# Kernel optimization log

Measured on AMD Instinct MI355X. Metric: run time of the kernel, lower is better.

## Reference

```python
import jax, jax.numpy as jnp
import numpy as np

B, T, N, H = 4, 10, 4096, 32
SR = 1.0  # sample_rate


def setup_inputs() -> dict:
    key = jax.random.key(0)
    ks = jax.random.split(key, 10)
    inputs = jax.random.normal(ks[0], (B, T, N), jnp.float32)
    states = jax.random.normal(ks[1], (T, B, N * H), jnp.float32) * 0.1
    dtw = jax.random.uniform(ks[2], (N, N), dtype=jnp.float32)
    spec_lap = jax.random.uniform(ks[3], (N, N), dtype=jnp.float32)
    laplacian = jax.random.uniform(ks[4], (N, N), dtype=jnp.float32)
    time_delay = jax.random.uniform(ks[5], (N, N), dtype=jnp.float32) * T
    W1 = jax.random.normal(ks[6], (H + 1, 2 * H), jnp.float32) * 0.05
    b1 = jnp.ones((2 * H,), jnp.float32)  # bias_init 1.0 for gate conv
    W2 = jax.random.normal(ks[7], (H + 1, H), jnp.float32) * 0.05
    b2 = jnp.zeros((H,), jnp.float32)
    return dict(inputs=inputs, states=states, dtw=dtw, spec_lap=spec_lap,
                laplacian=laplacian, time_delay=time_delay,
                W1=W1, b1=b1, W2=W2, b2=b2)


def _graph_conv(A, x, h, W, b):
    # x: [B,N], h: [B,N*H], A: [N,N] -> [B, N*out]
    conc = jnp.concatenate([x[:, :, None], h.reshape(B, N, H)], axis=2)  # [B,N,H+1]
    ac = jnp.einsum('mn,bnk->bmk', A, conc)                              # [B,N,H+1]
    out = ac @ W + b                                                     # [B,N,out]
    return out.reshape(B, -1)


def reference(inputs, states, dtw, spec_lap, laplacian, time_delay, W1, b1, W2, b2):
    eye = jnp.eye(N, dtype=jnp.float32)
    td = jnp.ceil(jnp.abs(time_delay) / SR)
    time_indicator = jnp.float32(T) - td  # tm - td with tm = times

    def step(carry, xs):
        gcn1, gcn2, _ = carry
        t, x_t, h_t = xs
        # time-based masking of dtw entries
        dtwt = jnp.where((dtw != 0) & (t + 1.0 > time_indicator), dtw, 0.0)
        multi = t == jnp.float32(T - 1)
        A = jnp.where(multi,
                      (dtwt + eye + laplacian + spec_lap) / 3.0,
                      (dtwt + spec_lap + eye) / 2.0)
        gcn1 = gcn1 + _graph_conv(A, x_t, h_t, W1, b1)       # [B, N*2H] (accumulated)
        ru = jax.nn.sigmoid(gcn1)
        r, u = jnp.split(ru, 2, axis=1)                      # flat split, as torch.chunk
        gcn2 = gcn2 + _graph_conv(A, x_t, r * h_t, W2, b2)   # [B, N*H]
        c = jnp.tanh(gcn2)
        h_new = u * h_t + (1.0 - u) * c
        return (gcn1, gcn2, h_new), None

    gcn1_0 = jnp.zeros((B, N * 2 * H), jnp.float32)
    gcn2_0 = jnp.zeros((B, N * H), jnp.float32)
    h0 = jnp.zeros((B, N * H), jnp.float32)
    ts = jnp.arange(T, dtype=jnp.float32)
    xs = (ts, jnp.transpose(inputs, (1, 0, 2)), states)  # per-step (t, x_t[B,N], h_t[B,N*H])
    (_, _, h_new), _ = jax.lax.scan(step, (gcn1_0, gcn2_0, h0), xs)
    return h_new  # [B, N*H]
```

## Files before the change

kernel.cpp:

```cpp
#include <hip/hip_runtime.h>
#include <math.h>

#define BB 4
#define TT 10
#define NN 4096
#define HH 32
#define JP 144
#define NJ2 (NN*JP)
#define NH (NN*HH)
#define NPAIR (NN*NN/2)

typedef __attribute__((ext_vector_type(8))) short short8;
typedef __attribute__((ext_vector_type(8))) _Float16 half8;
typedef __attribute__((ext_vector_type(4))) float floatx4;
typedef __attribute__((ext_vector_type(4))) unsigned int uintx4;
typedef __attribute__((ext_vector_type(2))) unsigned int uintx2;

__device__ inline unsigned short f2h(float f) {
    _Float16 h = (_Float16)f;
    unsigned short u; __builtin_memcpy(&u, &h, 2);
    return u;
}
__device__ inline unsigned pk2(float a, float b) {
    return (unsigned)f2h(a) | ((unsigned)f2h(b) << 16);
}

__global__ void k_pack(const float* __restrict__ dtw, const float* __restrict__ tdl,
                       const float* __restrict__ spl, const float* __restrict__ lap,
                       unsigned* __restrict__ Aoff, unsigned* __restrict__ Aon,
                       unsigned* __restrict__ A9, unsigned short* __restrict__ thr2) {
    int e = blockIdx.x * 256 + threadIdx.x;
    if (e >= NPAIR) return;
    size_t gi = (size_t)e * 2;
    int row = (int)(gi >> 12);
    int c0 = (int)(gi & 4095);
    float2 d = ((const float2*)dtw)[e];
    float2 td = ((const float2*)tdl)[e];
    float2 s = ((const float2*)spl)[e];
    float2 l = ((const float2*)lap)[e];
    float td0 = ceilf(fabsf(td.x)), td1 = ceilf(fabsf(td.y));
    int th0 = 10 - (int)td0; if (th0 < 0) th0 = 0;
    int th1 = 10 - (int)td1; if (th1 < 0) th1 = 0;
    float off0 = s.x + ((row == c0) ? 1.f : 0.f);
    float off1 = s.y + ((row == c0 + 1) ? 1.f : 0.f);
    float on0 = off0 + d.x, on1 = off1 + d.y;
    float a90 = off0 + l.x + ((td0 > 0.f && d.x != 0.f) ? d.x : 0.f);
    float a91 = off1 + l.y + ((td1 > 0.f && d.y != 0.f) ? d.y : 0.f);
    Aoff[e] = pk2(off0, off1);
    Aon[e]  = pk2(on0, on1);
    A9[e]   = pk2(a90, a91);
    thr2[e] = (unsigned short)(th0 | (th1 << 8));
}

__global__ void k_zpad(unsigned short* __restrict__ Ct) {
    int e = blockIdx.x * 256 + threadIdx.x;
    if (e >= TT * 12 * NN) return;
    int n = e & 4095;
    int r = e >> 12;
    int t = r / 12, j = 132 + (r % 12);
    Ct[(size_t)(t * JP + j) * NN + n] = 0;
}

__global__ void k_build_ct1(const float* __restrict__ inp, const float* __restrict__ st,
                            unsigned short* __restrict__ Ct) {
    int nb = blockIdx.x, b = blockIdx.y, t = blockIdx.z;
    int tid = threadIdx.x;
    float sc = (t == TT - 1) ? (1.f / 3.f) : 0.5f;
    int kk = tid & 31;
    int ng = tid >> 5;
    const float* stb = st + (size_t)(t * BB + b) * NH;
    unsigned short* crow = Ct + (size_t)(t * JP + b * 33 + 1 + kk) * NN;
    int n0 = nb * 128 + ng * 16;
#pragma unroll
    for (int i = 0; i < 16; i++) {
        int n = n0 + i;
        crow[n] = f2h(stb[n * 32 + kk] * sc);
    }
    if (tid < 128) {
        int n = nb * 128 + tid;
        Ct[(size_t)(t * JP + b * 33) * NN + n] = f2h(inp[((size_t)b * TT + t) * NN + n] * sc);
    }
}

__global__ void k_build_ct2(const float* __restrict__ inp, const float* __restrict__ st,
                            const float* __restrict__ G, unsigned short* __restrict__ Ct) {
    int nb = blockIdx.x, b = blockIdx.y, t = blockIdx.z;
    int tid = threadIdx.x;
    float sc = (t == TT - 1) ? (1.f / 3.f) : 0.5f;
    int kk = tid & 31;
    int ng = tid >> 5;
    const float* stb = st + (size_t)(t * BB + b) * NH;
    const float* Gb = G + (size_t)(t * BB + b) * NN * 64;
    unsigned short* crow = Ct + (size_t)(t * JP + b * 33 + 1 + kk) * NN;
    int n0 = nb * 128 + ng * 16;
#pragma unroll
    for (int i = 0; i < 16; i++) {
        int n = n0 + i;
        int jj = n * 32 + kk;
        float g = Gb[jj];
        float r = 1.0f / (1.0f + expf(-g));
        crow[n] = f2h(r * stb[jj] * sc);
    }
    if (tid < 128) {
        int n = nb * 128 + tid;
        Ct[(size_t)(t * JP + b * 33) * NN + n] = f2h(inp[((size_t)b * TT + t) * NN + n] * sc);
    }
}

__global__ __launch_bounds__(256) void k_mfma(const unsigned* __restrict__ Aoff,
                                              const unsigned* __restrict__ Aon,
                                              const unsigned* __restrict__ A9,
                                              const unsigned short* __restrict__ thr2,
                                              const unsigned* __restrict__ Ct,
                                              float* __restrict__ Out) {
    int t = blockIdx.z;
    int ks = blockIdx.y;
    int m0 = blockIdx.x * 128;
    int k0 = ks * 2048;
    int tid = threadIdx.x;
    int w = tid >> 6, lane = tid & 63;
    int lm = lane & 15, q = lane >> 4;

    __shared__ short As[128 * 40];
    __shared__ short Cs[JP * 40];
    unsigned* Asu = (unsigned*)As;
    unsigned* Csu = (unsigned*)Cs;

    floatx4 acc[2][9];
#pragma unroll
    for (int i = 0; i < 2; i++)
#pragma unroll
        for (int j = 0; j < 9; j++) acc[i][j] = (floatx4){0.f, 0.f, 0.f, 0.f};

    bool last = (t == TT - 1);

    for (int kb = 0; kb < 2048; kb += 32) {
        size_t kc = (size_t)(k0 + kb) >> 1;
#pragma unroll
        for (int it = 0; it < 2; it++) {
            int l = tid + 256 * it;
            int row = l >> 2, c4 = (l & 3) * 4;
            size_t g = (size_t)(m0 + row) * 2048 + kc + c4;
            uintx4 res;
            if (last) {
                res = *(const uintx4*)(A9 + g);
            } else {
                uintx4 o4 = *(const uintx4*)(Aoff + g);
                uintx4 a4 = *(const uintx4*)(Aon + g);
                uintx2 th2 = *(const uintx2*)(thr2 + g);
#pragma unroll
                for (int u = 0; u < 4; u++) {
                    unsigned th = (u < 2) ? (th2[0] >> ((u & 1) * 16)) : (th2[1] >> ((u & 1) * 16));
                    th &= 0xFFFFu;
                    unsigned lo = ((int)(th & 255u) <= t) ? a4[u] : o4[u];
                    unsigned hi = ((int)(th >> 8) <= t) ? a4[u] : o4[u];
                    res[u] = (lo & 0xFFFFu) | (hi & 0xFFFF0000u);
                }
            }
            *(uintx4*)(Asu + row * 20 + c4) = res;
        }
        for (int l = tid; l < 576; l += 256) {
            int j = l >> 2, c4 = (l & 3) * 4;
            size_t g = (size_t)(t * JP + j) * 2048 + kc + c4;
            *(uintx4*)(Csu + j * 20 + c4) = *(const uintx4*)(Ct + g);
        }
        __syncthreads();
        short8 a0 = *(const short8*)(As + (w * 32 + lm) * 40 + q * 8);
        short8 a1 = *(const short8*)(As + (w * 32 + 16 + lm) * 40 + q * 8);
        half8 ah0 = __builtin_bit_cast(half8, a0);
        half8 ah1 = __builtin_bit_cast(half8, a1);
#pragma unroll
        for (int jt = 0; jt < 9; jt++) {
            short8 bv = *(const short8*)(Cs + (jt * 16 + lm) * 40 + q * 8);
            half8 bh = __builtin_bit_cast(half8, bv);
            acc[0][jt] = __builtin_amdgcn_mfma_f32_16x16x32_f16(ah0, bh, acc[0][jt], 0, 0, 0);
            acc[1][jt] = __builtin_amdgcn_mfma_f32_16x16x32_f16(ah1, bh, acc[1][jt], 0, 0, 0);
        }
        __syncthreads();
    }
    float* Ob = Out + ((size_t)ks * TT + t) * (size_t)NN * JP;
#pragma unroll
    for (int mt = 0; mt < 2; mt++) {
        int row = m0 + w * 32 + mt * 16 + q * 4;
#pragma unroll
        for (int jt = 0; jt < 9; jt++) {
            int col = jt * 16 + lm;
#pragma unroll
            for (int r = 0; r < 4; r++)
                Ob[(size_t)(row + r) * JP + col] = acc[mt][jt][r];
        }
    }
}

__global__ void k_prefix(float* __restrict__ O0, const float* __restrict__ O1) {
    int e = blockIdx.x * 256 + threadIdx.x;
    if (e >= NJ2) return;
    float run = 0.f;
#pragma unroll
    for (int t = 0; t < TT; t++) {
        run += O0[(size_t)t * NJ2 + e] + O1[(size_t)t * NJ2 + e];
        O0[(size_t)t * NJ2 + e] = run;
    }
}

__global__ __launch_bounds__(256) void k_gcn1(const float* __restrict__ P,
                                              const float* __restrict__ W1,
                                              const float* __restrict__ b1,
                                              float* __restrict__ G) {
    int m0 = blockIdx.x * 32;
    int b = blockIdx.y, t = blockIdx.z;
    int tid = threadIdx.x;
    __shared__ float Ws[33 * 64];
    __shared__ float Ps[32 * 33];
    for (int l = tid; l < 33 * 64; l += 256) Ws[l] = W1[l];
    for (int l = tid; l < 32 * 33; l += 256) {
        int mr = l / 33, kk = l - mr * 33;
        Ps[l] = P[(size_t)(t * NN + m0 + mr) * JP + b * 33 + kk];
    }
    __syncthreads();
    int qq = tid & 63, ms = tid >> 6;
    float bias = (float)(t + 1) * b1[qq];
    for (int mi = 0; mi < 8; mi++) {
        int ml = ms * 8 + mi;
        float a = bias;
#pragma unroll
        for (int kk = 0; kk < 33; kk++) a = fmaf(Ps[ml * 33 + kk], Ws[kk * 64 + qq], a);
        G[(size_t)((t * BB + b) * NN + m0 + ml) * 64 + qq] = a;
    }
}

__global__ void k_reduce(const float* __restrict__ O0, const float* __restrict__ O1,
                         float* __restrict__ S) {
    int e = blockIdx.x * 256 + threadIdx.x;
    if (e >= NJ2) return;
    float s = 0.f;
#pragma unroll
    for (int t = 0; t < TT; t++)
        s += O0[(size_t)t * NJ2 + e] + O1[(size_t)t * NJ2 + e];
    S[e] = s;
}

__global__ __launch_bounds__(256) void k_final(const float* __restrict__ S,
                                               const float* __restrict__ G,
                                               const float* __restrict__ st,
                                               const float* __restrict__ W2,
                                               const float* __restrict__ b2,
                                               float* __restrict__ out) {
    __shared__ float Ws[33 * 32];
    int tid = threadIdx.x;
    for (int l = tid; l < 33 * 32; l += 256) Ws[l] = W2[l];
    __syncthreads();
    int e = blockIdx.x * 256 + tid;
    int b = e >> 17;
    int jj = e & (NH - 1);
    int m = jj >> 5, q = jj & 31;
    float a = 10.0f * b2[q];
#pragma unroll
    for (int kk = 0; kk < 33; kk++) a = fmaf(S[m * JP + b * 33 + kk], Ws[kk * 32 + q], a);
    float c = tanhf(a);
    float gu = G[(size_t)((9 * BB + b) * NN + 2048 + (jj >> 6)) * 64 + (jj & 63)];
    float u = 1.0f / (1.0f + expf(-gu));
    float h = st[(size_t)(9 * BB + b) * NH + jj];
    out[e] = u * h + (1.0f - u) * c;
}

extern "C" void kernel_launch(void* const* d_in, const int* in_sizes, int n_in,
                              void* d_out, int out_size, void* d_ws, size_t ws_size,
                              hipStream_t stream) {
    const float* inp = (const float*)d_in[0];
    const float* st  = (const float*)d_in[1];
    const float* dtw = (const float*)d_in[2];
    const float* spl = (const float*)d_in[3];
    const float* lap = (const float*)d_in[4];
    const float* tdl = (const float*)d_in[5];
    const float* W1  = (const float*)d_in[6];
    const float* b1  = (const float*)d_in[7];
    const float* W2  = (const float*)d_in[8];
    const float* b2  = (const float*)d_in[9];
    float* out = (float*)d_out;

    char* W = (char*)d_ws;
    unsigned*       Aoff = (unsigned*)W;                     W += (size_t)NPAIR * 4;
    unsigned*       Aon  = (unsigned*)W;                     W += (size_t)NPAIR * 4;
    unsigned*       A9   = (unsigned*)W;                     W += (size_t)NPAIR * 4;
    unsigned short* thr2 = (unsigned short*)W;               W += (size_t)NPAIR * 2;
    unsigned short* Ct   = (unsigned short*)W;               W += (size_t)TT * JP * NN * 2;
    float*          O    = (float*)W;                        W += (size_t)2 * TT * NJ2 * 4;
    float*          G    = (float*)W;                        W += (size_t)TT * BB * NN * 64 * 4;
    float*          S    = (float*)W;                        W += (size_t)NJ2 * 4;
    float* O1 = O + (size_t)TT * NJ2;

    k_pack<<<NPAIR / 256, 256, 0, stream>>>(dtw, tdl, spl, lap, Aoff, Aon, A9, thr2);
    k_zpad<<<(TT * 12 * NN + 255) / 256, 256, 0, stream>>>(Ct);

    dim3 gbld(NN / 128, BB, TT);
    k_build_ct1<<<gbld, 256, 0, stream>>>(inp, st, Ct);

    dim3 gmm(NN / 128, 2, TT);
    k_mfma<<<gmm, 256, 0, stream>>>(Aoff, Aon, A9, thr2, (const unsigned*)Ct, O);

    k_prefix<<<NJ2 / 256, 256, 0, stream>>>(O, O1);

    dim3 ggcn(NN / 32, BB, TT);
    k_gcn1<<<ggcn, 256, 0, stream>>>(O, W1, b1, G);

    k_build_ct2<<<gbld, 256, 0, stream>>>(inp, st, G, Ct);

    k_mfma<<<gmm, 256, 0, stream>>>(Aoff, Aon, A9, thr2, (const unsigned*)Ct, O);

    k_reduce<<<NJ2 / 256, 256, 0, stream>>>(O, O1, S);

    k_final<<<(BB * NN * HH) / 256, 256, 0, stream>>>(S, G, st, W2, b2, out);
}
```

Baseline: 639.7 us.

## Register-prefetch next K chunk in MFMA kernel and fold zero padding into builders

The MFMA GEMM kernel now loads the next K-chunk of A and Ct tiles into registers right after the barrier, before issuing MFMAs on the current chunk, so global-load latency overlaps compute. The grid is flattened to 1D so that both K-split halves of the same M tile are scheduled next to each other, which may improve L2 reuse of Ct. The separate zero-padding kernel is removed and its writes are folded into the Ct build kernels, saving one launch. The prefetch raises register pressure, which could reduce occupancy.

After: 640.2 us. No clear change (+0.1%).

```diff
diff --git a/kernel.cpp b/kernel.cpp
--- a/kernel.cpp
+++ b/kernel.cpp
@@ -52,15 +52,6 @@
     thr2[e] = (unsigned short)(th0 | (th1 << 8));
 }
 
-__global__ void k_zpad(unsigned short* __restrict__ Ct) {
-    int e = blockIdx.x * 256 + threadIdx.x;
-    if (e >= TT * 12 * NN) return;
-    int n = e & 4095;
-    int r = e >> 12;
-    int t = r / 12, j = 132 + (r % 12);
-    Ct[(size_t)(t * JP + j) * NN + n] = 0;
-}
-
 __global__ void k_build_ct1(const float* __restrict__ inp, const float* __restrict__ st,
                             unsigned short* __restrict__ Ct) {
     int nb = blockIdx.x, b = blockIdx.y, t = blockIdx.z;
@@ -79,6 +70,9 @@
     if (tid < 128) {
         int n = nb * 128 + tid;
         Ct[(size_t)(t * JP + b * 33) * NN + n] = f2h(inp[((size_t)b * TT + t) * NN + n] * sc);
+#pragma unroll
+        for (int rr = 0; rr < 3; rr++)
+            Ct[(size_t)(t * JP + 132 + b * 3 + rr) * NN + n] = 0;
     }
 }
 
@@ -104,6 +98,9 @@
     if (tid < 128) {
         int n = nb * 128 + tid;
         Ct[(size_t)(t * JP + b * 33) * NN + n] = f2h(inp[((size_t)b * TT + t) * NN + n] * sc);
+#pragma unroll
+        for (int rr = 0; rr < 3; rr++)
+            Ct[(size_t)(t * JP + 132 + b * 3 + rr) * NN + n] = 0;
     }
 }
 
@@ -113,9 +110,11 @@
                                               const unsigned short* __restrict__ thr2,
                                               const unsigned* __restrict__ Ct,
                                               float* __restrict__ Out) {
-    int t = blockIdx.z;
-    int ks = blockIdx.y;
-    int m0 = blockIdx.x * 128;
+    int f = blockIdx.x;
+    int t = f >> 6;
+    int g = f & 63;
+    int m0 = (g >> 1) * 128;
+    int ks = g & 1;
     int k0 = ks * 2048;
     int tid = threadIdx.x;
     int w = tid >> 6, lane = tid & 63;
@@ -134,20 +133,46 @@
 
     bool last = (t == TT - 1);
 
+    int row0 = tid >> 2, c4 = (tid & 3) * 4;
+    size_t cb = (size_t)t * JP;
+
+    uintx4 rO0, rO1, rN0, rN1, rC0, rC1, rC2;
+    uintx2 rT0, rT1;
+
+#define LOAD_CHUNK(KB)                                                              \
+    do {                                                                            \
+        size_t kc = (size_t)(k0 + (KB)) >> 1;                                       \
+        size_t g0 = (size_t)(m0 + row0) * 2048 + kc + c4;                           \
+        size_t g1 = g0 + (size_t)64 * 2048;                                         \
+        if (last) {                                                                 \
+            rO0 = *(const uintx4*)(A9 + g0);                                        \
+            rO1 = *(const uintx4*)(A9 + g1);                                        \
+        } else {                                                                    \
+            rO0 = *(const uintx4*)(Aoff + g0);                                      \
+            rO1 = *(const uintx4*)(Aoff + g1);                                      \
+            rN0 = *(const uintx4*)(Aon + g0);                                       \
+            rN1 = *(const uintx4*)(Aon + g1);                                       \
+            rT0 = *(const uintx2*)(thr2 + g0);                                      \
+            rT1 = *(const uintx2*)(thr2 + g1);                                      \
+        }                                                                           \
+        rC0 = *(const uintx4*)(Ct + (cb + row0) * 2048 + kc + c4);                  \
+        rC1 = *(const uintx4*)(Ct + (cb + row0 + 64) * 2048 + kc + c4);             \
+        if (tid < 64) rC2 = *(const uintx4*)(Ct + (cb + row0 + 128) * 2048 + kc + c4); \
+    } while (0)
+
+    LOAD_CHUNK(0);
+
     for (int kb = 0; kb < 2048; kb += 32) {
-        size_t kc = (size_t)(k0 + kb) >> 1;
 #pragma unroll
         for (int it = 0; it < 2; it++) {
-            int l = tid + 256 * it;
-            int row = l >> 2, c4 = (l & 3) * 4;
-            size_t g = (size_t)(m0 + row) * 2048 + kc + c4;
+            int row = row0 + it * 64;
             uintx4 res;
             if (last) {
-                res = *(const uintx4*)(A9 + g);
+                res = it ? rO1 : rO0;
             } else {
-                uintx4 o4 = *(const uintx4*)(Aoff + g);
-                uintx4 a4 = *(const uintx4*)(Aon + g);
-                uintx2 th2 = *(const uintx2*)(thr2 + g);
+                uintx4 o4 = it ? rO1 : rO0;
+                uintx4 a4 = it ? rN1 : rN0;
+                uintx2 th2 = it ? rT1 : rT0;
 #pragma unroll
                 for (int u = 0; u < 4; u++) {
                     unsigned th = (u < 2) ? (th2[0] >> ((u & 1) * 16)) : (th2[1] >> ((u & 1) * 16));
@@ -159,12 +184,13 @@
             }
             *(uintx4*)(Asu + row * 20 + c4) = res;
         }
-        for (int l = tid; l < 576; l += 256) {
-            int j = l >> 2, c4 = (l & 3) * 4;
-            size_t g = (size_t)(t * JP + j) * 2048 + kc + c4;
-            *(uintx4*)(Csu + j * 20 + c4) = *(const uintx4*)(Ct + g);
-        }
+        *(uintx4*)(Csu + row0 * 20 + c4) = rC0;
+        *(uintx4*)(Csu + (row0 + 64) * 20 + c4) = rC1;
+        if (tid < 64) *(uintx4*)(Csu + (row0 + 128) * 20 + c4) = rC2;
         __syncthreads();
+
+        if (kb + 32 < 2048) LOAD_CHUNK(kb + 32);
+
         short8 a0 = *(const short8*)(As + (w * 32 + lm) * 40 + q * 8);
         short8 a1 = *(const short8*)(As + (w * 32 + 16 + lm) * 40 + q * 8);
         half8 ah0 = __builtin_bit_cast(half8, a0);
@@ -178,6 +204,8 @@
         }
         __syncthreads();
     }
+#undef LOAD_CHUNK
+
     float* Ob = Out + ((size_t)ks * TT + t) * (size_t)NN * JP;
 #pragma unroll
     for (int mt = 0; mt < 2; mt++) {
@@ -291,13 +319,11 @@
     float* O1 = O + (size_t)TT * NJ2;
 
     k_pack<<<NPAIR / 256, 256, 0, stream>>>(dtw, tdl, spl, lap, Aoff, Aon, A9, thr2);
-    k_zpad<<<(TT * 12 * NN + 255) / 256, 256, 0, stream>>>(Ct);
 
     dim3 gbld(NN / 128, BB, TT);
     k_build_ct1<<<gbld, 256, 0, stream>>>(inp, st, Ct);
 
-    dim3 gmm(NN / 128, 2, TT);
-    k_mfma<<<gmm, 256, 0, stream>>>(Aoff, Aon, A9, thr2, (const unsigned*)Ct, O);
+    k_mfma<<<640, 256, 0, stream>>>(Aoff, Aon, A9, thr2, (const unsigned*)Ct, O);
 
     k_prefix<<<NJ2 / 256, 256, 0, stream>>>(O, O1);
 
@@ -306,7 +332,7 @@
 
     k_build_ct2<<<gbld, 256, 0, stream>>>(inp, st, G, Ct);
 
-    k_mfma<<<gmm, 256, 0, stream>>>(Aoff, Aon, A9, thr2, (const unsigned*)Ct, O);
+    k_mfma<<<640, 256, 0, stream>>>(Aoff, Aon, A9, thr2, (const unsigned*)Ct, O);
 
     k_reduce<<<NJ2 / 256, 256, 0, stream>>>(O, O1, S);
 
```
